# Kernel optimization log

Hardware: AMD Instinct MI355X
Metric: run time of the kernel (lower is better)

## Reference

```python
import jax, jax.numpy as jnp
import numpy as np

K = 16          # buckets per codeblock (2**treeDepth)
DEPTH = 4       # tree depth
C = 256         # codeblockCount
IN_FEATURES = 4096
OUT_FEATURES = 4096
N_ROWS = 4096

_BASE_TREE = np.array([
    [-1,-1,0,-1,0,0,0,-1,0,0,0,0,0,0,0],[-1,-1,0,-1,0,0,0,1,0,0,0,0,0,0,0],
    [-1,-1,0,1,0,0,0,0,-1,0,0,0,0,0,0],[-1,-1,0,1,0,0,0,0,1,0,0,0,0,0,0],
    [-1,1,0,0,-1,0,0,0,0,-1,0,0,0,0,0],[-1,1,0,0,-1,0,0,0,0,1,0,0,0,0,0],
    [-1,1,0,0,1,0,0,0,0,0,-1,0,0,0,0],[-1,1,0,0,1,0,0,0,0,0,1,0,0,0,0],
    [1,0,-1,0,0,-1,0,0,0,0,0,-1,0,0,0],[1,0,-1,0,0,-1,0,0,0,0,0,1,0,0,0],
    [1,0,-1,0,0,1,0,0,0,0,0,0,-1,0,0],[1,0,-1,0,0,1,0,0,0,0,0,0,1,0,0],
    [1,0,1,0,0,0,-1,0,0,0,0,0,0,-1,0],[1,0,1,0,0,0,-1,0,0,0,0,0,0,1,0],
    [1,0,1,0,0,0,1,0,0,0,0,0,0,0,-1],[1,0,1,0,0,0,1,0,0,0,0,0,0,0,1]],
    dtype=np.float32)

def _make_tree_des_matrix(c):
    # NOTE: original code initializes with ONES, then overwrites diagonal blocks
    m = np.ones((c * K, c * (K - 1)), dtype=np.float32)
    for i in range(c):
        m[i*K:(i+1)*K, i*(K-1):(i+1)*(K-1)] = _BASE_TREE
    return m

def _make_selection_matrix(c):
    base = np.zeros((K - 1, DEPTH), dtype=np.float32)
    base[0, 0] = 1.0
    for i in range(1, K - 1):
        base[i, int(np.log2(i + 1))] = 1.0
    m = np.zeros((c * (K - 1), c * DEPTH), dtype=np.float32)
    for i in range(c):
        m[i*(K-1):(i+1)*(K-1), i*DEPTH:(i+1)*DEPTH] = base
    return m

def setup_inputs() -> dict:
    key = jax.random.key(0)
    k1, k2, k3, k4 = jax.random.split(key, 4)
    inputMatrix = jax.random.normal(k1, (N_ROWS, IN_FEATURES), dtype=jnp.float32)
    dims = jax.random.randint(k2, (C * DEPTH,), 0, IN_FEATURES)
    selection_matrix = jnp.asarray(_make_selection_matrix(C))
    thresholds = jax.random.normal(k3, (C * (K - 1), 1), dtype=jnp.float32)
    tree_des_mat = jnp.asarray(_make_tree_des_matrix(C))
    lut = jax.random.normal(k4, (OUT_FEATURES, C, K), dtype=jnp.float32)
    return {"inputMatrix": inputMatrix, "dims": dims,
            "selection_matrix": selection_matrix, "thresholds": thresholds,
            "tree_des_mat": tree_des_mat, "lut": lut}

def reference(inputMatrix, dims, selection_matrix, thresholds, tree_des_mat, lut):
    n = inputMatrix.shape[0]
    c = lut.shape[1]
    # gather the tree-split feature dims: (N, C*DEPTH)
    chosen = inputMatrix[:, dims]
    # (C*15, N)
    subtracted = selection_matrix @ chosen.T - thresholds
    tanh_h = jnp.tanh(subtracted)
    sign_ste = jnp.sign(subtracted) - jax.lax.stop_gradient(tanh_h) + tanh_h
    # (C*16, N) -> (N, C, 16)
    tree_result = (tree_des_mat @ sign_ste).T.reshape(n, c, K)
    encoding_soft = jax.nn.softmax(tree_result, axis=2)
    index = jnp.argmax(encoding_soft, axis=2)
    encoding_hard = jax.nn.one_hot(index, K, dtype=encoding_soft.dtype)
    Encoded = encoding_hard - jax.lax.stop_gradient(encoding_soft) + encoding_soft
    # LUT lookup: einsum 'nij,kij->nki' + sum over i, fused to 'nij,kij->nk'
    out = jnp.einsum('nij,kij->nk', Encoded, lut)
    return out
```

## Files before the change

### kernel.cpp

```cpp
#include <hip/hip_runtime.h>

#define N_ROWS 4096
#define IN_F   4096
#define OUT_F  4096
#define C_CB   256
#define KDIM   4096

typedef short bf16x8 __attribute__((ext_vector_type(8)));
typedef float f32x4  __attribute__((ext_vector_type(4)));

union ABFrag { unsigned long long u[2]; bf16x8 v; };

__device__ __forceinline__ unsigned int f2bf(float f) {
    unsigned int u = __builtin_bit_cast(unsigned int, f);
    return (u + 0x7FFFu + ((u >> 16) & 1u)) >> 16;
}

__global__ __launch_bounds__(256) void k_idx(const float* __restrict__ input,
                                             const int* __restrict__ dims,
                                             const float* __restrict__ thr,
                                             unsigned char* __restrict__ idx4) {
    __shared__ float rowS[IN_F];
    __shared__ float thrS[C_CB * 15];
    __shared__ int   dimS[C_CB * 4];
    const int n = blockIdx.x;
    const int t = threadIdx.x;

    #pragma unroll
    for (int i = 0; i < 4; i++) dimS[i * 256 + t] = dims[i * 256 + t];
    #pragma unroll
    for (int i = 0; i < 15; i++) thrS[i * 256 + t] = thr[i * 256 + t];
    const float* row = input + (size_t)n * IN_F;
    #pragma unroll
    for (int i = 0; i < 4; i++) {
        float4 v = *(const float4*)(row + i * 1024 + t * 4);
        *(float4*)(rowS + i * 1024 + t * 4) = v;
    }
    __syncthreads();

    const int c = t;
    int4 d = *(const int4*)(dimS + c * 4);
    const float* th = thrS + c * 15;
    float x0 = rowS[d.x], x1 = rowS[d.y], x2 = rowS[d.z], x3 = rowS[d.w];
    int b0 = x0 > th[0];
    int j1 = 1 + b0;
    int b1 = x1 > th[j1];
    int j2 = 2 * j1 + 1 + b1;
    int b2 = x2 > th[j2];
    int j3 = 2 * j2 + 1 + b2;
    int b3 = x3 > th[j3];
    int idx = (b0 << 3) | (b1 << 2) | (b2 << 1) | b3;
    int other = __shfl_xor(idx, 1);
    if (!(c & 1))
        idx4[(c >> 1) * N_ROWS + n] = (unsigned char)(idx | (other << 4));
}

__global__ void k_cvt(const float* __restrict__ lut, unsigned short* __restrict__ lutb) {
    const int i = (blockIdx.x * blockDim.x + threadIdx.x) * 8;
    float4 a = *(const float4*)(lut + i);
    float4 b = *(const float4*)(lut + i + 4);
    uint4 o;
    o.x = f2bf(a.x) | (f2bf(a.y) << 16);
    o.y = f2bf(a.z) | (f2bf(a.w) << 16);
    o.z = f2bf(b.x) | (f2bf(b.y) << 16);
    o.w = f2bf(b.z) | (f2bf(b.w) << 16);
    *(uint4*)(lutb + i) = o;
}

#define BM 128
#define BN 128
#define BKT 64
#define BSTAGE (BN * BKT * 2)
#define NT (KDIM / BKT)

template<bool STAGE_FP32>
__global__ __launch_bounds__(256, 4) void k_gemm(const unsigned short* __restrict__ lutb,
                                                 const float* __restrict__ lutf,
                                                 const unsigned char* __restrict__ idx4,
                                                 float* __restrict__ out) {
    __shared__ unsigned char smem[8192 + 2 * BSTAGE];
    unsigned char* ish  = smem;
    unsigned char* bsh0 = smem + 8192;
    unsigned char* bsh1 = smem + 8192 + BSTAGE;

    const int t   = threadIdx.x;
    const int l15 = t & 15;
    const int q   = (t >> 4) & 3;
    const int w   = t >> 6;
    const int wm  = w >> 1, wn = w & 1;

    const int bid = blockIdx.x;
    const int bx  = ((bid & 7) << 2) | ((bid >> 3) & 3);
    const int by  = bid >> 5;
    const int m0  = by * BM;
    const int n0  = bx * BN;

    auto stageIdx = [&](int h) {
        #pragma unroll
        for (int qq = 0; qq < 2; qq++) {
            int L = qq * 256 + t;
            const unsigned char* g = idx4 + (size_t)(h * 64 + (L >> 3)) * N_ROWS + m0 + (L & 7) * 16;
            __builtin_amdgcn_global_load_lds(
                (const __attribute__((address_space(1))) void*)g,
                (__attribute__((address_space(3))) void*)(ish + L * 16), 16, 0, 0);
        }
    };

    auto stageB = [&](unsigned char* dst, int kbn) {
        #pragma unroll
        for (int qq = 0; qq < 4; qq++) {
            int L = qq * 256 + t;
            int r = L >> 3, p = L & 7;
            int c = p ^ (r & 7);
            const unsigned short* g = lutb + (size_t)(n0 + r) * KDIM + kbn + c * 8;
            __builtin_amdgcn_global_load_lds(
                (const __attribute__((address_space(1))) void*)g,
                (__attribute__((address_space(3))) void*)(dst + L * 16), 16, 0, 0);
        }
    };
    auto stageB32 = [&](unsigned char* dst, int kbn) {
        #pragma unroll
        for (int qq = 0; qq < 4; qq++) {
            int L = qq * 256 + t;
            int r = L >> 3, p = L & 7;
            int c = p ^ (r & 7);
            const float* g = lutf + (size_t)(n0 + r) * KDIM + kbn + c * 8;
            float4 f0 = *(const float4*)g;
            float4 f1 = *(const float4*)(g + 4);
            uint4 o;
            o.x = f2bf(f0.x) | (f2bf(f0.y) << 16);
            o.y = f2bf(f0.z) | (f2bf(f0.w) << 16);
            o.z = f2bf(f1.x) | (f2bf(f1.y) << 16);
            o.w = f2bf(f1.z) | (f2bf(f1.w) << 16);
            *(uint4*)(dst + L * 16) = o;
        }
    };

    f32x4 acc[4][4];
    #pragma unroll
    for (int mi = 0; mi < 4; mi++)
        #pragma unroll
        for (int ni = 0; ni < 4; ni++)
            acc[mi][ni] = (f32x4){0.f, 0.f, 0.f, 0.f};

    const int xorv = l15 & 7;
    const int bRowByte = (wn * 64 + l15) * (BKT * 2);
    const int aByte = wm * 64 + l15 * 4;
    const int qh4  = (q >> 1) * 4;
    const unsigned int sub8 = (q & 1) << 3;

    auto mfmaTile = [&](const unsigned char* src, int kb) {
        ABFrag bf2[2][4];
        unsigned int w32v[2];
        #pragma unroll
        for (int s = 0; s < 2; s++) {
            const int chunkOff = ((s * 4 + q) ^ xorv) * 16;
            #pragma unroll
            for (int ni = 0; ni < 4; ni++)
                bf2[s][ni].v = *(const bf16x8*)(src + bRowByte + ni * (16 * BKT * 2) + chunkOff);
            w32v[s] = *(const unsigned int*)(ish + ((((kb >> 5) + s) & 63) * 128) + aByte);
        }
        return [=](f32x4 (&ac)[4][4]) {
            #pragma unroll
            for (int s = 0; s < 2; s++) {
                ABFrag af[4];
                #pragma unroll
                for (int mi = 0; mi < 4; mi++) {
                    unsigned int T = (w32v[s] >> (mi * 8 + qh4)) & 0xFu;
                    unsigned int rel = T - sub8;
                    unsigned long long sh = 0x3F80ull << ((rel & 3) << 4);
                    af[mi].u[0] = (rel < 4u) ? sh : 0ull;
                    af[mi].u[1] = ((rel - 4u) < 4u) ? sh : 0ull;
                }
                #pragma unroll
                for (int mi = 0; mi < 4; mi++)
                    #pragma unroll
                    for (int ni = 0; ni < 4; ni++)
                        ac[mi][ni] = __builtin_amdgcn_mfma_f32_16x16x32_bf16(
                            af[mi].v, bf2[s][ni].v, ac[mi][ni], 0, 0, 0);
            }
        };
    };

    if (!STAGE_FP32) {
        stageIdx(0);
        stageB(bsh0, 0);
        stageB(bsh1, BKT);
        asm volatile("s_waitcnt vmcnt(4)" ::: "memory");
        __builtin_amdgcn_s_barrier();
        __builtin_amdgcn_sched_barrier(0);

        unsigned char* cur = bsh0;
        unsigned char* nxt = bsh1;
        for (int tt = 0; tt < NT; tt++) {
            const int kb = tt * BKT;
            auto doMfma = mfmaTile(cur, kb);
            asm volatile("s_waitcnt lgkmcnt(0)" ::: "memory");
            __builtin_amdgcn_s_barrier();
            __builtin_amdgcn_sched_barrier(0);
            if (tt == 31) stageIdx(1);
            if (tt + 2 < NT) stageB(cur, kb + 2 * BKT);
            __builtin_amdgcn_sched_barrier(0);
            __builtin_amdgcn_s_setprio(1);
            doMfma(acc);
            __builtin_amdgcn_s_setprio(0);
            if (tt + 2 < NT) asm volatile("s_waitcnt vmcnt(4)" ::: "memory");
            else             asm volatile("s_waitcnt vmcnt(0)" ::: "memory");
            __builtin_amdgcn_s_barrier();
            __builtin_amdgcn_sched_barrier(0);
            unsigned char* tmp = cur; cur = nxt; nxt = tmp;
        }
    } else {
        stageIdx(0);
        asm volatile("s_waitcnt vmcnt(0)" ::: "memory");
        __syncthreads();
        for (int tt = 0; tt < NT; tt++) {
            const int kb = tt * BKT;
            if (tt == 32) stageIdx(1);
            stageB32(bsh0, kb);
            __syncthreads();
            auto doMfma = mfmaTile(bsh0, kb);
            doMfma(acc);
            __syncthreads();
        }
    }

    #pragma unroll
    for (int mi = 0; mi < 4; mi++) {
        #pragma unroll
        for (int ni = 0; ni < 4; ni++) {
            const int col = n0 + wn * 64 + ni * 16 + l15;
            #pragma unroll
            for (int r = 0; r < 4; r++) {
                const int row = m0 + wm * 64 + 4 * (q * 4 + r) + mi;
                out[(size_t)row * OUT_F + col] = acc[mi][ni][r];
            }
        }
    }
}

extern "C" void kernel_launch(void* const* d_in, const int* in_sizes, int n_in,
                              void* d_out, int out_size, void* d_ws, size_t ws_size,
                              hipStream_t stream) {
    const float* input = (const float*)d_in[0];
    const int*   dims  = (const int*)d_in[1];
    const float* thr   = (const float*)d_in[3];
    const float* lut   = (const float*)d_in[5];
    float* out = (float*)d_out;

    const size_t lutbBytes = (size_t)OUT_F * KDIM * 2;
    const size_t idxBytes  = (size_t)(C_CB / 2) * N_ROWS;

    const int nblocks = (OUT_F / BN) * (N_ROWS / BM);

    if (ws_size >= lutbBytes + idxBytes) {
        unsigned short* lutb = (unsigned short*)d_ws;
        unsigned char*  idx4 = (unsigned char*)d_ws + lutbBytes;
        k_idx<<<N_ROWS, C_CB, 0, stream>>>(input, dims, thr, idx4);
        k_cvt<<<(OUT_F * KDIM) / (256 * 8), 256, 0, stream>>>(lut, lutb);
        k_gemm<false><<<nblocks, 256, 0, stream>>>(lutb, lut, idx4, out);
    } else {
        unsigned char* idx4 = (unsigned char*)d_ws;
        k_idx<<<N_ROWS, C_CB, 0, stream>>>(input, dims, thr, idx4);
        k_gemm<true><<<nblocks, 256, 0, stream>>>(nullptr, lut, idx4, out);
    }
}
```

Baseline: 297.4 us.

## Fuse LUT bf16 conversion into GEMM with register-staged prefetch and 256-row tiles

Removes the separate LUT fp32-to-bf16 conversion kernel and its bf16 workspace. The GEMM now loads fp32 LUT tiles into registers one iteration ahead, converts them with a perm-based packing, and writes them to LDS. Each block now covers two 128-row M tiles, so every converted B tile is reused twice and the whole index block (32KB) is staged once up front. In exchange, occupancy drops to 2 blocks per SM, the kernel reads twice the B bytes as fp32, and the asynchronous global-to-LDS B loads are replaced by register staging.

After: 302.1 us. No clear change (+1.6%).

```diff
diff --git a/kernel.cpp b/kernel.cpp
--- a/kernel.cpp
+++ b/kernel.cpp
@@ -11,9 +11,12 @@
 
 union ABFrag { unsigned long long u[2]; bf16x8 v; };
 
-__device__ __forceinline__ unsigned int f2bf(float f) {
-    unsigned int u = __builtin_bit_cast(unsigned int, f);
-    return (u + 0x7FFFu + ((u >> 16) & 1u)) >> 16;
+__device__ __forceinline__ unsigned int bfpack(float a, float b) {
+    unsigned int ua = __builtin_bit_cast(unsigned int, a);
+    unsigned int ub = __builtin_bit_cast(unsigned int, b);
+    ua += 0x7FFFu + ((ua >> 16) & 1u);
+    ub += 0x7FFFu + ((ub >> 16) & 1u);
+    return __builtin_amdgcn_perm(ub, ua, 0x07060302u);
 }
 
 __global__ __launch_bounds__(256) void k_idx(const float* __restrict__ input,
@@ -55,33 +58,20 @@
         idx4[(c >> 1) * N_ROWS + n] = (unsigned char)(idx | (other << 4));
 }
 
-__global__ void k_cvt(const float* __restrict__ lut, unsigned short* __restrict__ lutb) {
-    const int i = (blockIdx.x * blockDim.x + threadIdx.x) * 8;
-    float4 a = *(const float4*)(lut + i);
-    float4 b = *(const float4*)(lut + i + 4);
-    uint4 o;
-    o.x = f2bf(a.x) | (f2bf(a.y) << 16);
-    o.y = f2bf(a.z) | (f2bf(a.w) << 16);
-    o.z = f2bf(b.x) | (f2bf(b.y) << 16);
-    o.w = f2bf(b.z) | (f2bf(b.w) << 16);
-    *(uint4*)(lutb + i) = o;
-}
-
 #define BM 128
+#define MT 2
 #define BN 128
 #define BKT 64
 #define BSTAGE (BN * BKT * 2)
 #define NT (KDIM / BKT)
 
-template<bool STAGE_FP32>
-__global__ __launch_bounds__(256, 4) void k_gemm(const unsigned short* __restrict__ lutb,
-                                                 const float* __restrict__ lutf,
+__global__ __launch_bounds__(256, 2) void k_gemm(const float* __restrict__ lutf,
                                                  const unsigned char* __restrict__ idx4,
                                                  float* __restrict__ out) {
-    __shared__ unsigned char smem[8192 + 2 * BSTAGE];
+    __shared__ unsigned char smem[32768 + 2 * BSTAGE];
     unsigned char* ish  = smem;
-    unsigned char* bsh0 = smem + 8192;
-    unsigned char* bsh1 = smem + 8192 + BSTAGE;
+    unsigned char* bsh0 = smem + 32768;
+    unsigned char* bsh1 = smem + 32768 + BSTAGE;
 
     const int t   = threadIdx.x;
     const int l15 = t & 15;
@@ -91,82 +81,107 @@
 
     const int bid = blockIdx.x;
     const int bx  = ((bid & 7) << 2) | ((bid >> 3) & 3);
-    const int by  = bid >> 5;
-    const int m0  = by * BM;
+    const int byp = bid >> 5;
+    const int m0  = byp * (BM * MT);
     const int n0  = bx * BN;
 
-    auto stageIdx = [&](int h) {
-        #pragma unroll
-        for (int qq = 0; qq < 2; qq++) {
+    auto stageIdx = [&]() {
+        #pragma unroll
+        for (int qq = 0; qq < 8; qq++) {
             int L = qq * 256 + t;
-            const unsigned char* g = idx4 + (size_t)(h * 64 + (L >> 3)) * N_ROWS + m0 + (L & 7) * 16;
+            const unsigned char* g = idx4 + (size_t)(L >> 4) * N_ROWS + m0 + (L & 15) * 16;
             __builtin_amdgcn_global_load_lds(
                 (const __attribute__((address_space(1))) void*)g,
                 (__attribute__((address_space(3))) void*)(ish + L * 16), 16, 0, 0);
         }
     };
 
-    auto stageB = [&](unsigned char* dst, int kbn) {
-        #pragma unroll
-        for (int qq = 0; qq < 4; qq++) {
-            int L = qq * 256 + t;
-            int r = L >> 3, p = L & 7;
-            int c = p ^ (r & 7);
-            const unsigned short* g = lutb + (size_t)(n0 + r) * KDIM + kbn + c * 8;
-            __builtin_amdgcn_global_load_lds(
-                (const __attribute__((address_space(1))) void*)g,
-                (__attribute__((address_space(3))) void*)(dst + L * 16), 16, 0, 0);
-        }
-    };
-    auto stageB32 = [&](unsigned char* dst, int kbn) {
-        #pragma unroll
-        for (int qq = 0; qq < 4; qq++) {
-            int L = qq * 256 + t;
+    auto loadB = [&](float4* ra, int kbn) {
+        #pragma unroll
+        for (int i = 0; i < 4; i++) {
+            int L = i * 256 + t;
             int r = L >> 3, p = L & 7;
             int c = p ^ (r & 7);
             const float* g = lutf + (size_t)(n0 + r) * KDIM + kbn + c * 8;
-            float4 f0 = *(const float4*)g;
-            float4 f1 = *(const float4*)(g + 4);
+            ra[2 * i]     = *(const float4*)g;
+            ra[2 * i + 1] = *(const float4*)(g + 4);
+        }
+    };
+    auto cvtWrite = [&](unsigned char* dst, const float4* ra) {
+        #pragma unroll
+        for (int i = 0; i < 4; i++) {
+            float4 f0 = ra[2 * i], f1 = ra[2 * i + 1];
             uint4 o;
-            o.x = f2bf(f0.x) | (f2bf(f0.y) << 16);
-            o.y = f2bf(f0.z) | (f2bf(f0.w) << 16);
-            o.z = f2bf(f1.x) | (f2bf(f1.y) << 16);
-            o.w = f2bf(f1.z) | (f2bf(f1.w) << 16);
-            *(uint4*)(dst + L * 16) = o;
+            o.x = bfpack(f0.x, f0.y);
+            o.y = bfpack(f0.z, f0.w);
+            o.z = bfpack(f1.x, f1.y);
+            o.w = bfpack(f1.z, f1.w);
+            *(uint4*)(dst + (i * 256 + t) * 16) = o;
         }
     };
 
-    f32x4 acc[4][4];
-    #pragma unroll
-    for (int mi = 0; mi < 4; mi++)
-        #pragma unroll
-        for (int ni = 0; ni < 4; ni++)
-            acc[mi][ni] = (f32x4){0.f, 0.f, 0.f, 0.f};
+    f32x4 acc[MT][4][4];
+    #pragma unroll
+    for (int mt = 0; mt < MT; mt++)
+        #pragma unroll
+        for (int mi = 0; mi < 4; mi++)
+            #pragma unroll
+            for (int ni = 0; ni < 4; ni++)
+                acc[mt][mi][ni] = (f32x4){0.f, 0.f, 0.f, 0.f};
 
     const int xorv = l15 & 7;
     const int bRowByte = (wn * 64 + l15) * (BKT * 2);
     const int aByte = wm * 64 + l15 * 4;
+
     const int qh4  = (q >> 1) * 4;
     const unsigned int sub8 = (q & 1) << 3;
 
-    auto mfmaTile = [&](const unsigned char* src, int kb) {
+    float4 ra[8];
+
+    stageIdx();
+    loadB(ra, 0);
+    asm volatile("s_waitcnt vmcnt(0)" ::: "memory");
+    cvtWrite(bsh0, ra);
+    loadB(ra, BKT);
+    asm volatile("s_waitcnt vmcnt(0)" ::: "memory");
+    cvtWrite(bsh1, ra);
+    asm volatile("s_waitcnt lgkmcnt(0)" ::: "memory");
+    __builtin_amdgcn_s_barrier();
+    __builtin_amdgcn_sched_barrier(0);
+
+    for (int tt = 0; tt < NT; tt++) {
+        const int kb = tt * BKT;
+        unsigned char* cur = (tt & 1) ? bsh1 : bsh0;
+
         ABFrag bf2[2][4];
-        unsigned int w32v[2];
+        unsigned int w32v[2][MT];
         #pragma unroll
         for (int s = 0; s < 2; s++) {
             const int chunkOff = ((s * 4 + q) ^ xorv) * 16;
             #pragma unroll
             for (int ni = 0; ni < 4; ni++)
-                bf2[s][ni].v = *(const bf16x8*)(src + bRowByte + ni * (16 * BKT * 2) + chunkOff);
-            w32v[s] = *(const unsigned int*)(ish + ((((kb >> 5) + s) & 63) * 128) + aByte);
-        }
-        return [=](f32x4 (&ac)[4][4]) {
-            #pragma unroll
-            for (int s = 0; s < 2; s++) {
+                bf2[s][ni].v = *(const bf16x8*)(cur + bRowByte + ni * (16 * BKT * 2) + chunkOff);
+            #pragma unroll
+            for (int mt = 0; mt < MT; mt++)
+                w32v[s][mt] = *(const unsigned int*)(ish + ((kb >> 5) + s) * 256 + mt * 128 + aByte);
+        }
+        asm volatile("s_waitcnt lgkmcnt(0)" ::: "memory");
+        __builtin_amdgcn_sched_barrier(0);
+        __builtin_amdgcn_s_barrier();
+        __builtin_amdgcn_sched_barrier(0);
+        if (tt + 2 < NT) {
+            loadB(ra, kb + 2 * BKT);
+            __builtin_amdgcn_sched_barrier(0);
+        }
+        __builtin_amdgcn_s_setprio(1);
+        #pragma unroll
+        for (int s = 0; s < 2; s++) {
+            #pragma unroll
+            for (int mt = 0; mt < MT; mt++) {
                 ABFrag af[4];
                 #pragma unroll
                 for (int mi = 0; mi < 4; mi++) {
-                    unsigned int T = (w32v[s] >> (mi * 8 + qh4)) & 0xFu;
+                    unsigned int T = (w32v[s][mt] >> (mi * 8 + qh4)) & 0xFu;
                     unsigned int rel = T - sub8;
                     unsigned long long sh = 0x3F80ull << ((rel & 3) << 4);
                     af[mi].u[0] = (rel < 4u) ? sh : 0ull;
@@ -176,64 +191,33 @@
                 for (int mi = 0; mi < 4; mi++)
                     #pragma unroll
                     for (int ni = 0; ni < 4; ni++)
-                        ac[mi][ni] = __builtin_amdgcn_mfma_f32_16x16x32_bf16(
-                            af[mi].v, bf2[s][ni].v, ac[mi][ni], 0, 0, 0);
+                        acc[mt][mi][ni] = __builtin_amdgcn_mfma_f32_16x16x32_bf16(
+                            af[mi].v, bf2[s][ni].v, acc[mt][mi][ni], 0, 0, 0);
             }
-        };
-    };
-
-    if (!STAGE_FP32) {
-        stageIdx(0);
-        stageB(bsh0, 0);
-        stageB(bsh1, BKT);
-        asm volatile("s_waitcnt vmcnt(4)" ::: "memory");
+        }
+        __builtin_amdgcn_s_setprio(0);
+        __builtin_amdgcn_sched_barrier(0);
+        if (tt + 2 < NT) {
+            asm volatile("s_waitcnt vmcnt(0)" ::: "memory");
+            cvtWrite(cur, ra);
+            asm volatile("s_waitcnt lgkmcnt(0)" ::: "memory");
+        }
         __builtin_amdgcn_s_barrier();
         __builtin_amdgcn_sched_barrier(0);
-
-        unsigned char* cur = bsh0;
-        unsigned char* nxt = bsh1;
-        for (int tt = 0; tt < NT; tt++) {
-            const int kb = tt * BKT;
-            auto doMfma = mfmaTile(cur, kb);
-            asm volatile("s_waitcnt lgkmcnt(0)" ::: "memory");
-            __builtin_amdgcn_s_barrier();
-            __builtin_amdgcn_sched_barrier(0);
-            if (tt == 31) stageIdx(1);
-            if (tt + 2 < NT) stageB(cur, kb + 2 * BKT);
-            __builtin_amdgcn_sched_barrier(0);
-            __builtin_amdgcn_s_setprio(1);
-            doMfma(acc);
-            __builtin_amdgcn_s_setprio(0);
-            if (tt + 2 < NT) asm volatile("s_waitcnt vmcnt(4)" ::: "memory");
-            else             asm volatile("s_waitcnt vmcnt(0)" ::: "memory");
-            __builtin_amdgcn_s_barrier();
-            __builtin_amdgcn_sched_barrier(0);
-            unsigned char* tmp = cur; cur = nxt; nxt = tmp;
-        }
-    } else {
-        stageIdx(0);
-        asm volatile("s_waitcnt vmcnt(0)" ::: "memory");
-        __syncthreads();
-        for (int tt = 0; tt < NT; tt++) {
-            const int kb = tt * BKT;
-            if (tt == 32) stageIdx(1);
-            stageB32(bsh0, kb);
-            __syncthreads();
-            auto doMfma = mfmaTile(bsh0, kb);
-            doMfma(acc);
-            __syncthreads();
-        }
     }
 
     #pragma unroll
-    for (int mi = 0; mi < 4; mi++) {
-        #pragma unroll
-        for (int ni = 0; ni < 4; ni++) {
-            const int col = n0 + wn * 64 + ni * 16 + l15;
-            #pragma unroll
-            for (int r = 0; r < 4; r++) {
-                const int row = m0 + wm * 64 + 4 * (q * 4 + r) + mi;
-                out[(size_t)row * OUT_F + col] = acc[mi][ni][r];
+    for (int mt = 0; mt < MT; mt++) {
+        #pragma unroll
+        for (int mi = 0; mi < 4; mi++) {
+            #pragma unroll
+            for (int ni = 0; ni < 4; ni++) {
+                const int col = n0 + wn * 64 + ni * 16 + l15;
+                #pragma unroll
+                for (int r = 0; r < 4; r++) {
+                    const int row = m0 + mt * 128 + wm * 64 + 4 * (q * 4 + r) + mi;
+                    out[(size_t)row * OUT_F + col] = acc[mt][mi][ni][r];
+                }
             }
         }
     }
@@ -248,20 +232,10 @@
     const float* lut   = (const float*)d_in[5];
     float* out = (float*)d_out;
 
-    const size_t lutbBytes = (size_t)OUT_F * KDIM * 2;
-    const size_t idxBytes  = (size_t)(C_CB / 2) * N_ROWS;
-
-    const int nblocks = (OUT_F / BN) * (N_ROWS / BM);
-
-    if (ws_size >= lutbBytes + idxBytes) {
-        unsigned short* lutb = (unsigned short*)d_ws;
-        unsigned char*  idx4 = (unsigned char*)d_ws + lutbBytes;
-        k_idx<<<N_ROWS, C_CB, 0, stream>>>(input, dims, thr, idx4);
-        k_cvt<<<(OUT_F * KDIM) / (256 * 8), 256, 0, stream>>>(lut, lutb);
-        k_gemm<false><<<nblocks, 256, 0, stream>>>(lutb, lut, idx4, out);
-    } else {
-        unsigned char* idx4 = (unsigned char*)d_ws;
-        k_idx<<<N_ROWS, C_CB, 0, stream>>>(input, dims, thr, idx4);
-        k_gemm<true><<<nblocks, 256, 0, stream>>>(nullptr, lut, idx4, out);
-    }
-}
+    unsigned char* idx4 = (unsigned char*)d_ws;
+
+    const int nblocks = (OUT_F / BN) * (N_ROWS / (BM * MT));
+
+    k_idx<<<N_ROWS, C_CB, 0, stream>>>(input, dims, thr, idx4);
+    k_gemm<<<nblocks, 256, 0, stream>>>(lut, idx4, out);
+}
```

## Widen GEMM N-tile to 256 and split LDS reads into two overlapped phases

Applied to the files above, without the earlier changes.

Doubles the block's N tile from 128 to 256, so each warp computes a 64x128 output slab with twice as many accumulators, and cuts occupancy from 4 to 2 blocks per CU. This amortizes the index decode and LDS A-fragment work over more MFMAs and halves the number of blocks re-reading the idx buffer. The inner loop is also restructured so the second k-half's LDS reads are issued while the first half's MFMAs run. The cost is higher register pressure, a larger LDS footprint and fewer waves to hide latency.

Result: faster. 284.7 us (-4.3%).

```diff
diff --git a/kernel.cpp b/kernel.cpp
--- a/kernel.cpp
+++ b/kernel.cpp
@@ -68,13 +68,13 @@
 }
 
 #define BM 128
-#define BN 128
+#define BN 256
 #define BKT 64
 #define BSTAGE (BN * BKT * 2)
 #define NT (KDIM / BKT)
 
 template<bool STAGE_FP32>
-__global__ __launch_bounds__(256, 4) void k_gemm(const unsigned short* __restrict__ lutb,
+__global__ __launch_bounds__(256, 2) void k_gemm(const unsigned short* __restrict__ lutb,
                                                  const float* __restrict__ lutf,
                                                  const unsigned char* __restrict__ idx4,
                                                  float* __restrict__ out) {
@@ -90,8 +90,8 @@
     const int wm  = w >> 1, wn = w & 1;
 
     const int bid = blockIdx.x;
-    const int bx  = ((bid & 7) << 2) | ((bid >> 3) & 3);
-    const int by  = bid >> 5;
+    const int bx  = ((bid & 7) << 1) | ((bid >> 3) & 1);
+    const int by  = bid >> 4;
     const int m0  = by * BM;
     const int n0  = bx * BN;
 
@@ -108,7 +108,7 @@
 
     auto stageB = [&](unsigned char* dst, int kbn) {
         #pragma unroll
-        for (int qq = 0; qq < 4; qq++) {
+        for (int qq = 0; qq < 8; qq++) {
             int L = qq * 256 + t;
             int r = L >> 3, p = L & 7;
             int c = p ^ (r & 7);
@@ -120,7 +120,7 @@
     };
     auto stageB32 = [&](unsigned char* dst, int kbn) {
         #pragma unroll
-        for (int qq = 0; qq < 4; qq++) {
+        for (int qq = 0; qq < 8; qq++) {
             int L = qq * 256 + t;
             int r = L >> 3, p = L & 7;
             int c = p ^ (r & 7);
@@ -136,75 +136,77 @@
         }
     };
 
-    f32x4 acc[4][4];
+    f32x4 acc[4][8];
     #pragma unroll
     for (int mi = 0; mi < 4; mi++)
         #pragma unroll
-        for (int ni = 0; ni < 4; ni++)
+        for (int ni = 0; ni < 8; ni++)
             acc[mi][ni] = (f32x4){0.f, 0.f, 0.f, 0.f};
 
     const int xorv = l15 & 7;
-    const int bRowByte = (wn * 64 + l15) * (BKT * 2);
+    const int bRowByte = (wn * 128 + l15) * (BKT * 2);
     const int aByte = wm * 64 + l15 * 4;
     const int qh4  = (q >> 1) * 4;
     const unsigned int sub8 = (q & 1) << 3;
 
-    auto mfmaTile = [&](const unsigned char* src, int kb) {
-        ABFrag bf2[2][4];
-        unsigned int w32v[2];
-        #pragma unroll
-        for (int s = 0; s < 2; s++) {
-            const int chunkOff = ((s * 4 + q) ^ xorv) * 16;
+    auto readPhase = [&](const unsigned char* src, int s, int kb, ABFrag (&bf)[8], unsigned int& w32) {
+        const int chunkOff = ((s * 4 + q) ^ xorv) * 16;
+        #pragma unroll
+        for (int ni = 0; ni < 8; ni++)
+            bf[ni].v = *(const bf16x8*)(src + bRowByte + ni * (16 * BKT * 2) + chunkOff);
+        w32 = *(const unsigned int*)(ish + ((((kb >> 5) + s) & 63) * 128) + aByte);
+    };
+    auto mfmaPhase = [&](const ABFrag (&bf)[8], unsigned int w32) {
+        ABFrag af[4];
+        #pragma unroll
+        for (int mi = 0; mi < 4; mi++) {
+            unsigned int T = (w32 >> (mi * 8 + qh4)) & 0xFu;
+            unsigned int rel = T - sub8;
+            unsigned long long sh = 0x3F80ull << ((rel & 3) << 4);
+            af[mi].u[0] = (rel < 4u) ? sh : 0ull;
+            af[mi].u[1] = ((rel - 4u) < 4u) ? sh : 0ull;
+        }
+        #pragma unroll
+        for (int mi = 0; mi < 4; mi++)
             #pragma unroll
-            for (int ni = 0; ni < 4; ni++)
-                bf2[s][ni].v = *(const bf16x8*)(src + bRowByte + ni * (16 * BKT * 2) + chunkOff);
-            w32v[s] = *(const unsigned int*)(ish + ((((kb >> 5) + s) & 63) * 128) + aByte);
-        }
-        return [=](f32x4 (&ac)[4][4]) {
-            #pragma unroll
-            for (int s = 0; s < 2; s++) {
-                ABFrag af[4];
-                #pragma unroll
-                for (int mi = 0; mi < 4; mi++) {
-                    unsigned int T = (w32v[s] >> (mi * 8 + qh4)) & 0xFu;
-                    unsigned int rel = T - sub8;
-                    unsigned long long sh = 0x3F80ull << ((rel & 3) << 4);
-                    af[mi].u[0] = (rel < 4u) ? sh : 0ull;
-                    af[mi].u[1] = ((rel - 4u) < 4u) ? sh : 0ull;
-                }
-                #pragma unroll
-                for (int mi = 0; mi < 4; mi++)
-                    #pragma unroll
-                    for (int ni = 0; ni < 4; ni++)
-                        ac[mi][ni] = __builtin_amdgcn_mfma_f32_16x16x32_bf16(
-                            af[mi].v, bf2[s][ni].v, ac[mi][ni], 0, 0, 0);
-            }
-        };
+            for (int ni = 0; ni < 8; ni++)
+                acc[mi][ni] = __builtin_amdgcn_mfma_f32_16x16x32_bf16(
+                    af[mi].v, bf[ni].v, acc[mi][ni], 0, 0, 0);
     };
 
     if (!STAGE_FP32) {
         stageIdx(0);
         stageB(bsh0, 0);
         stageB(bsh1, BKT);
-        asm volatile("s_waitcnt vmcnt(4)" ::: "memory");
+        asm volatile("s_waitcnt vmcnt(8)" ::: "memory");
         __builtin_amdgcn_s_barrier();
         __builtin_amdgcn_sched_barrier(0);
 
         unsigned char* cur = bsh0;
         unsigned char* nxt = bsh1;
+        ABFrag bf0[8], bf1[8];
+        unsigned int w0, w1;
         for (int tt = 0; tt < NT; tt++) {
             const int kb = tt * BKT;
-            auto doMfma = mfmaTile(cur, kb);
+            readPhase(cur, 0, kb, bf0, w0);
             asm volatile("s_waitcnt lgkmcnt(0)" ::: "memory");
+            __builtin_amdgcn_sched_barrier(0);
+            readPhase(cur, 1, kb, bf1, w1);
+            __builtin_amdgcn_sched_barrier(0);
+            __builtin_amdgcn_s_setprio(1);
+            mfmaPhase(bf0, w0);
+            __builtin_amdgcn_s_setprio(0);
+            asm volatile("s_waitcnt lgkmcnt(0)" ::: "memory");
+            __builtin_amdgcn_sched_barrier(0);
             __builtin_amdgcn_s_barrier();
             __builtin_amdgcn_sched_barrier(0);
             if (tt == 31) stageIdx(1);
             if (tt + 2 < NT) stageB(cur, kb + 2 * BKT);
             __builtin_amdgcn_sched_barrier(0);
             __builtin_amdgcn_s_setprio(1);
-            doMfma(acc);
+            mfmaPhase(bf1, w1);
             __builtin_amdgcn_s_setprio(0);
-            if (tt + 2 < NT) asm volatile("s_waitcnt vmcnt(4)" ::: "memory");
+            if (tt + 2 < NT) asm volatile("s_waitcnt vmcnt(8)" ::: "memory");
             else             asm volatile("s_waitcnt vmcnt(0)" ::: "memory");
             __builtin_amdgcn_s_barrier();
             __builtin_amdgcn_sched_barrier(0);
@@ -214,13 +216,18 @@
         stageIdx(0);
         asm volatile("s_waitcnt vmcnt(0)" ::: "memory");
         __syncthreads();
+        ABFrag bfx[8];
+        unsigned int wx;
         for (int tt = 0; tt < NT; tt++) {
             const int kb = tt * BKT;
             if (tt == 32) stageIdx(1);
             stageB32(bsh0, kb);
             __syncthreads();
-            auto doMfma = mfmaTile(bsh0, kb);
-            doMfma(acc);
+            #pragma unroll
+            for (int s = 0; s < 2; s++) {
+                readPhase(bsh0, s, kb, bfx, wx);
+                mfmaPhase(bfx, wx);
+            }
             __syncthreads();
         }
     }
@@ -228,8 +235,8 @@
     #pragma unroll
     for (int mi = 0; mi < 4; mi++) {
         #pragma unroll
-        for (int ni = 0; ni < 4; ni++) {
-            const int col = n0 + wn * 64 + ni * 16 + l15;
+        for (int ni = 0; ni < 8; ni++) {
+            const int col = n0 + wn * 128 + ni * 16 + l15;
             #pragma unroll
             for (int r = 0; r < 4; r++) {
                 const int row = m0 + wm * 64 + 4 * (q * 4 + r) + mi;
```
